# Performance work log

Measured on AMD Instinct MI355X. Metric: run time of the kernel, lower is better.

## Reference

```python
import jax, jax.numpy as jnp
import numpy as np

EMBED_DIM = 1024
N_HEADS = 16
HEAD_DIM = EMBED_DIM // N_HEADS


def setup_inputs() -> dict:
    key = jax.random.key(0)
    k1, k2, k3 = jax.random.split(key, 3)
    B, T, D = 2, 2048, EMBED_DIM
    x = jax.random.normal(k1, (B, T, D), dtype=jnp.float32)
    # torch nn.Linear weights: (out_features, in_features); y = x @ W.T
    scale = 1.0 / np.sqrt(D)
    qkv_w = jax.random.uniform(k2, (3 * D, D), dtype=jnp.float32, minval=-scale, maxval=scale)
    out_w = jax.random.uniform(k3, (D, D), dtype=jnp.float32, minval=-scale, maxval=scale)
    return {"x": x, "qkv_w": qkv_w, "out_w": out_w}


def reference(x, qkv_w, out_w):
    B, T, D = x.shape
    H, hd = N_HEADS, HEAD_DIM
    qkv = jnp.einsum('btd,ed->bte', x, qkv_w)  # (B,T,3D)
    qkv = qkv.reshape(B, T, 3, H, hd)
    q = jnp.transpose(qkv[:, :, 0], (0, 2, 1, 3))  # (B,H,T,hd)
    k = jnp.transpose(qkv[:, :, 1], (0, 2, 1, 3))
    v = jnp.transpose(qkv[:, :, 2], (0, 2, 1, 3))
    scores = jnp.einsum('bhtd,bhsd->bhts', q, k) / np.sqrt(hd).astype(np.float32)
    causal = jnp.tril(jnp.ones((T, T), dtype=bool))  # True = keep
    scores = jnp.where(causal[None, None], scores, -jnp.inf)
    probs = jax.nn.softmax(scores, axis=-1)
    out = jnp.einsum('bhts,bhsd->bhtd', probs, v)
    out = jnp.transpose(out, (0, 2, 1, 3)).reshape(B, T, D)
    return jnp.einsum('btd,ed->bte', out, out_w)
```

## Files before the change

kernel.cpp:

```cpp
#include <hip/hip_runtime.h>
#include <hip/hip_bf16.h>
#include <stdint.h>

typedef __bf16 bf16;
typedef __attribute__((ext_vector_type(8))) __bf16 bf16x8;
typedef __attribute__((ext_vector_type(4))) __bf16 bf16x4;
typedef __attribute__((ext_vector_type(4))) float f32x4;
typedef __attribute__((ext_vector_type(16))) float f32x16;

#define AS1 __attribute__((address_space(1)))
#define AS3 __attribute__((address_space(3)))

__device__ __forceinline__ void async16(const void* g, void* l) {
  __builtin_amdgcn_global_load_lds((AS1 uint32_t*)(g), (AS3 uint32_t*)(l), 16, 0, 0);
}

__device__ __forceinline__ f32x4 mfma_bf16(bf16x8 a, bf16x8 b, f32x4 c) {
  return __builtin_amdgcn_mfma_f32_16x16x32_bf16(a, b, c, 0, 0, 0);
}

__device__ __forceinline__ f32x16 mfma32(bf16x8 a, bf16x8 b, f32x16 c) {
  return __builtin_amdgcn_mfma_f32_32x32x16_bf16(a, b, c, 0, 0, 0);
}

__device__ __forceinline__ uint32_t pack2_bf16(float a, float b) {
  union { __hip_bfloat162 h2; uint32_t u; } u;
  u.h2 = __float22bfloat162_rn(float2{a, b});
  return u.u;
}

__global__ __launch_bounds__(256) void cast_all_kernel(
    const float* __restrict__ x, const float* __restrict__ w1,
    const float* __restrict__ w2, bf16* __restrict__ xb,
    bf16* __restrict__ w1b, bf16* __restrict__ w2b) {
  const int bid = blockIdx.x;
  const float* src;
  bf16* dst;
  int base;
  if (bid < 4096) { src = x;  dst = xb;  base = bid; }
  else if (bid < 7168) { src = w1; dst = w1b; base = bid - 4096; }
  else { src = w2; dst = w2b; base = bid - 7168; }
  const int i = (base * 256 + threadIdx.x) * 4;
  const float4 v = *(const float4*)(src + i);
  bf16x4 o;
  o[0] = (bf16)v.x; o[1] = (bf16)v.y; o[2] = (bf16)v.z; o[3] = (bf16)v.w;
  *(bf16x4*)(dst + i) = o;
}

__global__ __launch_bounds__(256) void gemm_qkv_kernel(
    const bf16* __restrict__ A, const bf16* __restrict__ W,
    bf16* __restrict__ QK, bf16* __restrict__ VT) {
  constexpr int K = 1024;
  __shared__ __align__(16) bf16 sm[2 * 128 * 32];
  const int tid = threadIdx.x;
  const int w = tid >> 6, lane = tid & 63;
  const int m0 = blockIdx.x * 128, n0 = blockIdx.y * 128;
  const int wm = (w >> 1) * 64, wn = (w & 1) * 64;
  const int lrow = lane & 15, quad = lane >> 4;
  const int lk = quad * 8;
  f32x4 acc[4][4] = {};

  for (int k0 = 0; k0 < K; k0 += 32) {
#pragma unroll
    for (int i = 0; i < 4; ++i) {
      const int c = tid + 256 * i;
      const bf16* src = (c < 512)
          ? (A + (size_t)(m0 + (c >> 2)) * K + k0 + (c & 3) * 8)
          : (W + (size_t)(n0 + ((c - 512) >> 2)) * K + k0 + (c & 3) * 8);
      async16(src, sm + (w * 64 + i * 256) * 8);
    }
    __syncthreads();
    bf16x8 af[4], bfr[4];
#pragma unroll
    for (int mi = 0; mi < 4; ++mi)
      af[mi] = *(const bf16x8*)&sm[(wm + mi * 16 + lrow) * 32 + lk];
#pragma unroll
    for (int ni = 0; ni < 4; ++ni)
      bfr[ni] = *(const bf16x8*)&sm[128 * 32 + (wn + ni * 16 + lrow) * 32 + lk];
#pragma unroll
    for (int mi = 0; mi < 4; ++mi)
#pragma unroll
      for (int ni = 0; ni < 4; ++ni)
        acc[mi][ni] = mfma_bf16(af[mi], bfr[ni], acc[mi][ni]);
    __syncthreads();
  }

  bf16* s2 = sm;
  const bool isV = (n0 >= 2048);
  const int bb = m0 >> 11;
  const int mt = m0 & 2047;
  if (!isV) {
#pragma unroll
    for (int c = 0; c < 2; ++c) {
      if ((w >> 1) == c) {
#pragma unroll
        for (int mi = 0; mi < 4; ++mi)
#pragma unroll
          for (int ni = 0; ni < 4; ++ni) {
            const int nr = wn + ni * 16 + lrow;
#pragma unroll
            for (int r = 0; r < 4; ++r)
              s2[(mi * 16 + quad * 4 + r) * 128 + nr] = (bf16)acc[mi][ni][r];
          }
      }
      __syncthreads();
#pragma unroll
      for (int p = 0; p < 4; ++p) {
        const int row = p * 16 + (tid >> 4);
        const int colc = (tid & 15) * 8;
        const bf16x8 v = *(const bf16x8*)&s2[row * 128 + colc];
        *(bf16x8*)(QK + (size_t)(m0 + c * 64 + row) * 2048 + n0 + colc) = v;
      }
      __syncthreads();
    }
  } else {
#pragma unroll
    for (int c = 0; c < 2; ++c) {
      if ((w & 1) == c) {
#pragma unroll
        for (int mi = 0; mi < 4; ++mi)
#pragma unroll
          for (int ni = 0; ni < 4; ++ni) {
            const int nl = ni * 16 + lrow;
            bf16x4 pk4;
#pragma unroll
            for (int r = 0; r < 4; ++r) pk4[r] = (bf16)acc[mi][ni][r];
            *(bf16x4*)&s2[nl * 128 + wm + mi * 16 + quad * 4] = pk4;
          }
      }
      __syncthreads();
#pragma unroll
      for (int p = 0; p < 4; ++p) {
        const int row = p * 16 + (tid >> 4);
        const int colc = (tid & 15) * 8;
        const bf16x8 v = *(const bf16x8*)&s2[row * 128 + colc];
        const int vtrow = bb * 1024 + (n0 - 2048) + c * 64 + row;
        *(bf16x8*)(VT + (size_t)vtrow * 2048 + mt + colc) = v;
      }
      __syncthreads();
    }
  }
}

__global__ __launch_bounds__(256) void attn_kernel(
    const bf16* __restrict__ QK, const bf16* __restrict__ VT,
    bf16* __restrict__ AO) {
  __shared__ __align__(16) bf16 sK[2][2][64 * 64];
  __shared__ __align__(16) bf16 sV[2][2][64 * 64];
  const int bid = blockIdx.x;
  const int bh = bid & 31;
  const int bp = bid >> 5;
  const int b = bh >> 4, hd = bh & 15;
  const int tid = threadIdx.x, w = tid >> 6, lane = tid & 63;
  const int ln31 = lane & 31, hf = lane >> 5;
  const bf16* Qb = QK + (size_t)b * 2048 * 2048 + hd * 64;
  const bf16* Kb = Qb + 1024;
  const bf16* Vb = VT + (size_t)bh * 64 * 2048;
  const float NEG_INF = -__builtin_inff();
  constexpr float QSCALE = 0.18033688011112042f;
  const int n0 = 16 - bp;
  const int RH = (15 - bp) * 128 + w * 32;
  const int RL = bp * 128 + w * 32;

  union { uint32_t u[4]; bf16x8 v; } ones;
  ones.u[0] = 0x3F803F80u; ones.u[1] = 0x3F803F80u;
  ones.u[2] = 0x3F803F80u; ones.u[3] = 0x3F803F80u;

  bf16x8 qfH[4], qfL[4];
#pragma unroll
  for (int ks = 0; ks < 4; ++ks) {
    bf16x8 v0 = *(const bf16x8*)(Qb + (size_t)(RH + ln31) * 2048 + ks * 16 + hf * 8);
    bf16x8 v1 = *(const bf16x8*)(Qb + (size_t)(RL + ln31) * 2048 + ks * 16 + hf * 8);
#pragma unroll
    for (int e = 0; e < 8; ++e) {
      v0[e] = (bf16)((float)v0[e] * QSCALE);
      v1[e] = (bf16)((float)v1[e] * QSCALE);
    }
    qfH[ks] = v0; qfL[ks] = v1;
  }

  auto stage = [&](int s0, int c) {
    bf16* dK = &sK[c][0][0];
    bf16* dV = &sV[c][0][0];
#pragma unroll
    for (int i2 = 0; i2 < 4; ++i2) {
      const int L = tid + 256 * i2;
      const int buf = L >> 9, Lr = L & 511;
      const int row = Lr >> 3;
      const int ch = (Lr & 7) ^ (row & 7);
      async16(Kb + (size_t)(s0 + buf * 64 + row) * 2048 + ch * 8, dK + L * 8);
    }
#pragma unroll
    for (int i2 = 0; i2 < 4; ++i2) {
      const int L = tid + 256 * i2;
      const int buf = L >> 9, Lr = L & 511;
      const int d = Lr >> 3;
      const int ch = (Lr & 7) ^ (d & 7);
      async16(Vb + (size_t)d * 2048 + s0 + buf * 64 + ch * 8, dV + L * 8);
    }
  };

  f32x16 accO0 = {}, accO1 = {};
  f32x16 accL = {};

  auto body = [&](const bf16* kbuf, const bf16* vbuf, const bf16x8 (&qf)[4],
                  int kv0, int R, bool masked) {
    f32x16 st0 = {}, st1 = {};
#pragma unroll
    for (int ks = 0; ks < 4; ++ks) {
      const int ch = (((2 * ks + hf) ^ (ln31 & 7)) * 8);
      const bf16x8 kf0 = *(const bf16x8*)&kbuf[ln31 * 64 + ch];
      const bf16x8 kf1 = *(const bf16x8*)&kbuf[(32 + ln31) * 64 + ch];
      st0 = mfma32(kf0, qf[ks], st0);
      st1 = mfma32(kf1, qf[ks], st1);
    }
    const int q = R + ln31;
    float p0[16], p1[16];
#pragma unroll
    for (int r = 0; r < 16; ++r) {
      const int crow = (r & 3) + 8 * (r >> 2) + 4 * hf;
      float s0 = st0[r], s1 = st1[r];
      if (masked) {
        s0 = (kv0 + crow <= q) ? s0 : NEG_INF;
        s1 = (kv0 + 32 + crow <= q) ? s1 : NEG_INF;
      }
      p0[r] = __builtin_amdgcn_exp2f(s0);
      p1[r] = __builtin_amdgcn_exp2f(s1);
    }
    bf16x8 pa[4];
#pragma unroll
    for (int mt = 0; mt < 2; ++mt) {
#pragma unroll
      for (int ksl = 0; ksl < 2; ++ksl) {
        const int bs = ksl * 8;
        uint32_t x0, y0, x1, y1;
        if (mt == 0) {
          x0 = pack2_bf16(p0[bs + 0], p0[bs + 1]);
          y0 = pack2_bf16(p0[bs + 4], p0[bs + 5]);
          x1 = pack2_bf16(p0[bs + 2], p0[bs + 3]);
          y1 = pack2_bf16(p0[bs + 6], p0[bs + 7]);
        } else {
          x0 = pack2_bf16(p1[bs + 0], p1[bs + 1]);
          y0 = pack2_bf16(p1[bs + 4], p1[bs + 5]);
          x1 = pack2_bf16(p1[bs + 2], p1[bs + 3]);
          y1 = pack2_bf16(p1[bs + 6], p1[bs + 7]);
        }
        asm volatile("v_permlane32_swap_b32 %0, %1" : "+v"(x0), "+v"(y0));
        asm volatile("v_permlane32_swap_b32 %0, %1" : "+v"(x1), "+v"(y1));
        union { uint32_t u[4]; bf16x8 v; } f;
        f.u[0] = x0; f.u[1] = x1; f.u[2] = y0; f.u[3] = y1;
        pa[mt * 2 + ksl] = f.v;
      }
    }
#pragma unroll
    for (int ks = 0; ks < 4; ++ks) {
      const int ch = (((2 * ks + hf) ^ (ln31 & 7)) * 8);
      const bf16x8 vf0 = *(const bf16x8*)&vbuf[ln31 * 64 + ch];
      const bf16x8 vf1 = *(const bf16x8*)&vbuf[(32 + ln31) * 64 + ch];
      accO0 = mfma32(pa[ks], vf0, accO0);
      accO1 = mfma32(pa[ks], vf1, accO1);
      accL  = mfma32(pa[ks], ones.v, accL);
    }
  };

  auto writeout = [&](int R) {
    bf16* Ob = AO + (size_t)b * 2048 * 1024 + hd * 64;
#pragma unroll
    for (int r = 0; r < 16; ++r) {
      const int qr = R + (r & 3) + 8 * (r >> 2) + 4 * hf;
      const float inv = 1.0f / accL[r];
      Ob[(size_t)qr * 1024 + ln31]      = (bf16)(accO0[r] * inv);
      Ob[(size_t)qr * 1024 + 32 + ln31] = (bf16)(accO1[r] * inv);
    }
  };

  stage(0, 0);
  int cur = 0;
  for (int i = 0; i < 17; ++i) {
    if (i + 1 < 17) {
      const int nx = (i + 1 < n0) ? (i + 1) : (i + 1 - n0);
      stage(nx * 128, cur ^ 1);
      asm volatile("s_waitcnt vmcnt(8)" ::: "memory");
    } else {
      asm volatile("s_waitcnt vmcnt(0)" ::: "memory");
    }
    __builtin_amdgcn_s_barrier();
    if (i < n0) {
      const int kv0 = i * 128;
      if (kv0 <= RH + 31)
        body(&sK[cur][0][0], &sV[cur][0][0], qfH, kv0, RH, kv0 + 63 > RH);
      if (kv0 + 64 <= RH + 31)
        body(&sK[cur][1][0], &sV[cur][1][0], qfH, kv0 + 64, RH, kv0 + 127 > RH);
      if (i == n0 - 1) {
        writeout(RH);
        accO0 = f32x16{}; accO1 = f32x16{}; accL = f32x16{};
      }
    } else {
      const int kv0 = (i - n0) * 128;
      if (kv0 <= RL + 31)
        body(&sK[cur][0][0], &sV[cur][0][0], qfL, kv0, RL, kv0 + 63 > RL);
      if (kv0 + 64 <= RL + 31)
        body(&sK[cur][1][0], &sV[cur][1][0], qfL, kv0 + 64, RL, kv0 + 127 > RL);
    }
    __builtin_amdgcn_s_barrier();
    cur ^= 1;
  }
  writeout(RL);
}

__global__ __launch_bounds__(256) void gemm_out_kernel(
    const bf16* __restrict__ A, const bf16* __restrict__ W,
    float* __restrict__ C) {
  constexpr int K = 1024;
  __shared__ __align__(16) bf16 sm[2 * 128 * 32];
  const int tid = threadIdx.x;
  const int w = tid >> 6, lane = tid & 63;
  const int m0 = blockIdx.x * 128, n0 = blockIdx.y * 128;
  const int wm = (w >> 1) * 64, wn = (w & 1) * 64;
  const int lrow = lane & 15, lk = (lane >> 4) * 8;
  f32x4 acc[4][4] = {};

  for (int k0 = 0; k0 < K; k0 += 32) {
#pragma unroll
    for (int i = 0; i < 4; ++i) {
      const int c = tid + 256 * i;
      const bf16* src = (c < 512)
          ? (A + (size_t)(m0 + (c >> 2)) * K + k0 + (c & 3) * 8)
          : (W + (size_t)(n0 + ((c - 512) >> 2)) * K + k0 + (c & 3) * 8);
      async16(src, sm + (w * 64 + i * 256) * 8);
    }
    __syncthreads();
    bf16x8 af[4], bfr[4];
#pragma unroll
    for (int mi = 0; mi < 4; ++mi)
      af[mi] = *(const bf16x8*)&sm[(wm + mi * 16 + lrow) * 32 + lk];
#pragma unroll
    for (int ni = 0; ni < 4; ++ni)
      bfr[ni] = *(const bf16x8*)&sm[128 * 32 + (wn + ni * 16 + lrow) * 32 + lk];
#pragma unroll
    for (int mi = 0; mi < 4; ++mi)
#pragma unroll
      for (int ni = 0; ni < 4; ++ni)
        acc[mi][ni] = mfma_bf16(af[mi], bfr[ni], acc[mi][ni]);
    __syncthreads();
  }

#pragma unroll
  for (int mi = 0; mi < 4; ++mi)
#pragma unroll
    for (int ni = 0; ni < 4; ++ni) {
      const int n = n0 + wn + ni * 16 + lrow;
#pragma unroll
      for (int r = 0; r < 4; ++r) {
        const int m = m0 + wm + mi * 16 + (lane >> 4) * 4 + r;
        C[(size_t)m * 1024 + n] = acc[mi][ni][r];
      }
    }
}

extern "C" void kernel_launch(void* const* d_in, const int* in_sizes, int n_in,
                              void* d_out, int out_size, void* d_ws, size_t ws_size,
                              hipStream_t stream) {
  const float* x     = (const float*)d_in[0];
  const float* qkv_w = (const float*)d_in[1];
  const float* out_w = (const float*)d_in[2];
  float* out = (float*)d_out;

  char* ws = (char*)d_ws;
  bf16* xb    = (bf16*)(ws);
  bf16* aob   = (bf16*)(ws);
  bf16* wqkvb = (bf16*)(ws + 8u * 1024 * 1024);
  bf16* wob   = (bf16*)(ws + 14u * 1024 * 1024);
  bf16* qkb   = (bf16*)(ws + 16u * 1024 * 1024);
  bf16* vtb   = (bf16*)(ws + 32u * 1024 * 1024);

  cast_all_kernel<<<8192, 256, 0, stream>>>(x, qkv_w, out_w, xb, wqkvb, wob);
  gemm_qkv_kernel<<<dim3(32, 24), 256, 0, stream>>>(xb, wqkvb, qkb, vtb);
  attn_kernel<<<dim3(256), 256, 0, stream>>>(qkb, vtb, aob);
  gemm_out_kernel<<<dim3(32, 8), 256, 0, stream>>>(aob, wob, out);
}
```

Baseline: 196.0 us.

## Split attention KV halves across wave pairs with LDS reduction of partial outputs

Doubles the attention block to 512 threads so that each pair of waves handles the same 32 query rows, with one wave processing the first 64-key half and the other the second half of each 128-key tile. The partial O and row-sum accumulators are combined through LDS scratch (reusing the current K/V buffers) before the normalized write. This aims to raise parallelism and latency hiding, since only 256 blocks are launched. The cost is extra barriers and LDS traffic at each write-out. Reusing the live K/V buffer as scratch risks races with in-flight async loads into the other buffer.

```diff
diff --git a/kernel.cpp b/kernel.cpp
--- a/kernel.cpp
+++ b/kernel.cpp
@@ -142,7 +142,7 @@
   }
 }
 
-__global__ __launch_bounds__(256) void attn_kernel(
+__global__ __launch_bounds__(512) void attn_kernel(
     const bf16* __restrict__ QK, const bf16* __restrict__ VT,
     bf16* __restrict__ AO) {
   __shared__ __align__(16) bf16 sK[2][2][64 * 64];
@@ -152,6 +152,7 @@
   const int bp = bid >> 5;
   const int b = bh >> 4, hd = bh & 15;
   const int tid = threadIdx.x, w = tid >> 6, lane = tid & 63;
+  const int slice = w >> 1, parity = w & 1;
   const int ln31 = lane & 31, hf = lane >> 5;
   const bf16* Qb = QK + (size_t)b * 2048 * 2048 + hd * 64;
   const bf16* Kb = Qb + 1024;
@@ -159,8 +160,8 @@
   const float NEG_INF = -__builtin_inff();
   constexpr float QSCALE = 0.18033688011112042f;
   const int n0 = 16 - bp;
-  const int RH = (15 - bp) * 128 + w * 32;
-  const int RL = bp * 128 + w * 32;
+  const int RH = (15 - bp) * 128 + slice * 32;
+  const int RL = bp * 128 + slice * 32;
 
   union { uint32_t u[4]; bf16x8 v; } ones;
   ones.u[0] = 0x3F803F80u; ones.u[1] = 0x3F803F80u;
@@ -183,16 +184,16 @@
     bf16* dK = &sK[c][0][0];
     bf16* dV = &sV[c][0][0];
 #pragma unroll
-    for (int i2 = 0; i2 < 4; ++i2) {
-      const int L = tid + 256 * i2;
+    for (int i2 = 0; i2 < 2; ++i2) {
+      const int L = tid + 512 * i2;
       const int buf = L >> 9, Lr = L & 511;
       const int row = Lr >> 3;
       const int ch = (Lr & 7) ^ (row & 7);
       async16(Kb + (size_t)(s0 + buf * 64 + row) * 2048 + ch * 8, dK + L * 8);
     }
 #pragma unroll
-    for (int i2 = 0; i2 < 4; ++i2) {
-      const int L = tid + 256 * i2;
+    for (int i2 = 0; i2 < 2; ++i2) {
+      const int L = tid + 512 * i2;
       const int buf = L >> 9, Lr = L & 511;
       const int d = Lr >> 3;
       const int ch = (Lr & 7) ^ (d & 7);
@@ -203,7 +204,7 @@
   f32x16 accO0 = {}, accO1 = {};
   f32x16 accL = {};
 
-  auto body = [&](const bf16* kbuf, const bf16* vbuf, const bf16x8 (&qf)[4],
+  auto body = [&](const bf16* kbuf, const bf16* vbuf, const bf16x8* qf,
                   int kv0, int R, bool masked) {
     f32x16 st0 = {}, st1 = {};
 #pragma unroll
@@ -263,15 +264,43 @@
     }
   };
 
-  auto writeout = [&](int R) {
-    bf16* Ob = AO + (size_t)b * 2048 * 1024 + hd * 64;
-#pragma unroll
-    for (int r = 0; r < 16; ++r) {
-      const int qr = R + (r & 3) + 8 * (r >> 2) + 4 * hf;
-      const float inv = 1.0f / accL[r];
-      Ob[(size_t)qr * 1024 + ln31]      = (bf16)(accO0[r] * inv);
-      Ob[(size_t)qr * 1024 + 32 + ln31] = (bf16)(accO1[r] * inv);
-    }
+  auto combine_write = [&](int R, int cur) {
+    float* scrA = (float*)&sK[cur][0][0];
+    float* scrB = (float*)&sV[cur][0][0];
+    const int base = (slice * 64 + lane) * 16;
+    __builtin_amdgcn_s_barrier();
+    if (parity == 1) {
+#pragma unroll
+      for (int r = 0; r < 16; ++r) scrA[base + r] = accO0[r];
+#pragma unroll
+      for (int r = 0; r < 16; ++r) scrB[base + r] = accL[r];
+    }
+    __builtin_amdgcn_s_barrier();
+    if (parity == 0) {
+#pragma unroll
+      for (int r = 0; r < 16; ++r) accO0[r] += scrA[base + r];
+#pragma unroll
+      for (int r = 0; r < 16; ++r) accL[r] += scrB[base + r];
+    }
+    __builtin_amdgcn_s_barrier();
+    if (parity == 1) {
+#pragma unroll
+      for (int r = 0; r < 16; ++r) scrA[base + r] = accO1[r];
+    }
+    __builtin_amdgcn_s_barrier();
+    if (parity == 0) {
+#pragma unroll
+      for (int r = 0; r < 16; ++r) accO1[r] += scrA[base + r];
+      bf16* Ob = AO + (size_t)b * 2048 * 1024 + hd * 64;
+#pragma unroll
+      for (int r = 0; r < 16; ++r) {
+        const int qr = R + (r & 3) + 8 * (r >> 2) + 4 * hf;
+        const float inv = 1.0f / accL[r];
+        Ob[(size_t)qr * 1024 + ln31]      = (bf16)(accO0[r] * inv);
+        Ob[(size_t)qr * 1024 + 32 + ln31] = (bf16)(accO1[r] * inv);
+      }
+    }
+    accO0 = f32x16{}; accO1 = f32x16{}; accL = f32x16{};
   };
 
   stage(0, 0);
@@ -280,32 +309,23 @@
     if (i + 1 < 17) {
       const int nx = (i + 1 < n0) ? (i + 1) : (i + 1 - n0);
       stage(nx * 128, cur ^ 1);
-      asm volatile("s_waitcnt vmcnt(8)" ::: "memory");
+      asm volatile("s_waitcnt vmcnt(4)" ::: "memory");
     } else {
       asm volatile("s_waitcnt vmcnt(0)" ::: "memory");
     }
     __builtin_amdgcn_s_barrier();
-    if (i < n0) {
-      const int kv0 = i * 128;
-      if (kv0 <= RH + 31)
-        body(&sK[cur][0][0], &sV[cur][0][0], qfH, kv0, RH, kv0 + 63 > RH);
-      if (kv0 + 64 <= RH + 31)
-        body(&sK[cur][1][0], &sV[cur][1][0], qfH, kv0 + 64, RH, kv0 + 127 > RH);
-      if (i == n0 - 1) {
-        writeout(RH);
-        accO0 = f32x16{}; accO1 = f32x16{}; accL = f32x16{};
-      }
-    } else {
-      const int kv0 = (i - n0) * 128;
-      if (kv0 <= RL + 31)
-        body(&sK[cur][0][0], &sV[cur][0][0], qfL, kv0, RL, kv0 + 63 > RL);
-      if (kv0 + 64 <= RL + 31)
-        body(&sK[cur][1][0], &sV[cur][1][0], qfL, kv0 + 64, RL, kv0 + 127 > RL);
-    }
+    const bool inH = (i < n0);
+    const int j = inH ? i : i - n0;
+    const int R = inH ? RH : RL;
+    const int kv0 = j * 128 + parity * 64;
+    if (kv0 <= R + 31)
+      body(&sK[cur][parity][0], &sV[cur][parity][0],
+           inH ? qfH : qfL, kv0, R, kv0 + 63 > R);
+    if (i == n0 - 1) combine_write(RH, cur);
     __builtin_amdgcn_s_barrier();
     cur ^= 1;
   }
-  writeout(RL);
+  combine_write(RL, cur);
 }
 
 __global__ __launch_bounds__(256) void gemm_out_kernel(
@@ -376,6 +396,6 @@
 
   cast_all_kernel<<<8192, 256, 0, stream>>>(x, qkv_w, out_w, xb, wqkvb, wob);
   gemm_qkv_kernel<<<dim3(32, 24), 256, 0, stream>>>(xb, wqkvb, qkb, vtb);
-  attn_kernel<<<dim3(256), 256, 0, stream>>>(qkb, vtb, aob);
+  attn_kernel<<<dim3(256), 512, 0, stream>>>(qkb, vtb, aob);
   gemm_out_kernel<<<dim3(32, 8), 256, 0, stream>>>(aob, wob, out);
 }
```

After: 176.3 us. 1.11x faster.
